# Kernel optimization log

Measured on AMD Instinct MI355X. Metric: run time of the kernel, lower is better.

The kernel has to match this reference:

```python
import jax, jax.numpy as jnp
import numpy as np

N = 50000      # nodes
E = 400000     # edges (before self-loops)
DIN = 128
HID = 128
HEADS = 4
DOUT = 64
NEG_SLOPE = 0.2  # PyG GATConv default


def setup_inputs() -> dict:
    key = jax.random.key(0)
    ks = jax.random.split(key, 14)

    def w(k, shape, fan_in):
        return jax.random.normal(k, shape, dtype=jnp.float32) * (1.0 / np.sqrt(fan_in))

    x = jax.random.normal(ks[0], (N, DIN), dtype=jnp.float32)
    edge_index = jax.random.randint(ks[1], (2, E), 0, N, dtype=jnp.int32)

    # layer 1: DIN -> HEADS*HID (concat)
    W1 = w(ks[2], (DIN, HEADS * HID), DIN)
    a_src1 = w(ks[3], (HEADS, HID), HID)
    a_dst1 = w(ks[4], (HEADS, HID), HID)
    b1 = jnp.zeros((HEADS * HID,), jnp.float32)
    # layer 2: HEADS*HID -> HEADS*HID (concat)
    W2 = w(ks[5], (HEADS * HID, HEADS * HID), HEADS * HID)
    a_src2 = w(ks[6], (HEADS, HID), HID)
    a_dst2 = w(ks[7], (HEADS, HID), HID)
    b2 = jnp.zeros((HEADS * HID,), jnp.float32)
    # layer 3: HEADS*HID -> DOUT, heads=1, concat=False (mean)
    W3 = w(ks[8], (HEADS * HID, DOUT), HEADS * HID)
    a_src3 = w(ks[9], (1, DOUT), DOUT)
    a_dst3 = w(ks[10], (1, DOUT), DOUT)
    b3 = jnp.zeros((DOUT,), jnp.float32)

    return dict(x=x, edge_index=edge_index,
                W1=W1, a_src1=a_src1, a_dst1=a_dst1, b1=b1,
                W2=W2, a_src2=a_src2, a_dst2=a_dst2, b2=b2,
                W3=W3, a_src3=a_src3, a_dst3=a_dst3, b3=b3)


def _gat_layer(x, src, dst, W, a_src, a_dst, n):
    """One GATConv (eval mode, self-loops already in src/dst). Returns [n, H, C]."""
    H, C = a_src.shape
    h = (x @ W).reshape(n, H, C)                        # projected features
    alpha_s = jnp.einsum('nhc,hc->nh', h, a_src)        # per-node src logits
    alpha_d = jnp.einsum('nhc,hc->nh', h, a_dst)
    e = jax.nn.leaky_relu(alpha_s[src] + alpha_d[dst], NEG_SLOPE)  # [E', H]
    # segment softmax over incoming edges of each dst node
    m = jax.ops.segment_max(e, dst, num_segments=n)
    e = jnp.exp(e - m[dst])
    s = jax.ops.segment_sum(e, dst, num_segments=n)
    alpha = e / (s[dst] + 1e-16)                        # [E', H]
    msg = h[src] * alpha[:, :, None]                    # [E', H, C]
    return jax.ops.segment_sum(msg, dst, num_segments=n)


def reference(x, edge_index, W1, a_src1, a_dst1, b1,
              W2, a_src2, a_dst2, b2, W3, a_src3, a_dst3, b3):
    n = x.shape[0]
    loops = jnp.arange(n, dtype=edge_index.dtype)       # PyG add_self_loops=True
    src = jnp.concatenate([edge_index[0], loops])
    dst = jnp.concatenate([edge_index[1], loops])

    h = _gat_layer(x, src, dst, W1, a_src1, a_dst1, n).reshape(n, -1) + b1
    h = jax.nn.elu(h)   # dropout is identity in eval mode
    h = _gat_layer(h, src, dst, W2, a_src2, a_dst2, n).reshape(n, -1) + b2
    h = jax.nn.elu(h)
    out = _gat_layer(h, src, dst, W3, a_src3, a_dst3, n)[:, 0, :] + b3  # heads=1, concat=False
    return out
```

## Files before the change

### kernel.cpp

```cpp
#include <hip/hip_runtime.h>
#include <hip/hip_bf16.h>


typedef __attribute__((ext_vector_type(8))) short bf16x8;
typedef __attribute__((ext_vector_type(4))) float f32x4;

__device__ __forceinline__ float bflo(unsigned w) { return __uint_as_float(w << 16); }
__device__ __forceinline__ float bfhi(unsigned w) { return __uint_as_float(w & 0xffff0000u); }
__device__ __forceinline__ float leaky(float x) { return x > 0.f ? x : 0.2f * x; }


__global__ void k_count(const int* __restrict__ ei, int E, int N, int* __restrict__ cnt) {
    int e = blockIdx.x * blockDim.x + threadIdx.x;
    int tot = E + N;
    if (e >= tot) return;
    int d = (e < E) ? ei[E + e] : (e - E);
    atomicAdd(&cnt[d], 1);
}

__global__ void k_scan1(const int* __restrict__ cnt, int N, int* __restrict__ rp,
                        int* __restrict__ blksum) {
    __shared__ int sdata[256];
    int t = threadIdx.x;
    int base = blockIdx.x * 1024;
    int v[4];
    int loc = 0;
#pragma unroll
    for (int i = 0; i < 4; i++) {
        int idx = base + t * 4 + i;
        v[i] = (idx < N) ? cnt[idx] : 0;
        loc += v[i];
    }
    int x = loc;
    sdata[t] = x;
    __syncthreads();
    for (int off = 1; off < 256; off <<= 1) {
        int y = (t >= off) ? sdata[t - off] : 0;
        __syncthreads();
        x += y;
        sdata[t] = x;
        __syncthreads();
    }
    int run = x - loc;
#pragma unroll
    for (int i = 0; i < 4; i++) {
        int idx = base + t * 4 + i;
        if (idx < N) rp[idx] = run;
        run += v[i];
    }
    if (t == 255) blksum[blockIdx.x] = x;
}

__global__ void k_scan2(const int* __restrict__ blksum, int nblk, int* __restrict__ blkoff) {
    int l = threadIdx.x;
    int v = (l < nblk) ? blksum[l] : 0;
    int x = v;
#pragma unroll
    for (int off = 1; off < 64; off <<= 1) {
        int y = __shfl_up(x, off);
        if (l >= off) x += y;
    }
    if (l < nblk) blkoff[l] = x - v;
}

__global__ void k_scan3(int* __restrict__ rp, const int* __restrict__ blkoff, int N, int Etot,
                        int* __restrict__ cur) {
    int i = blockIdx.x * blockDim.x + threadIdx.x;
    if (i < N) {
        int v = rp[i] + blkoff[i >> 10];
        rp[i] = v;
        cur[i] = v;
    }
    if (i == 0) rp[N] = Etot;
}

__global__ void k_fill(const int* __restrict__ ei, int E, int N, int* __restrict__ cur,
                       int* __restrict__ col, int* __restrict__ dste) {
    int e = blockIdx.x * blockDim.x + threadIdx.x;
    int tot = E + N;
    if (e >= tot) return;
    int s, d;
    if (e < E) { s = ei[e]; d = ei[E + e]; }
    else       { s = e - E; d = e - E; }
    int p = atomicAdd(&cur[d], 1);
    col[p] = s;
    dste[p] = d;
}


__global__ void k_cast_pad(const float* __restrict__ X, __hip_bfloat16* __restrict__ Xb,
                           int n_elems, int total) {
    int i = (blockIdx.x * blockDim.x + threadIdx.x) * 4;
    if (i >= total) return;
    float4 v = make_float4(0.f, 0.f, 0.f, 0.f);
    if (i < n_elems) v = *(const float4*)&X[i];
    __hip_bfloat16 tmp[4] = {__float2bfloat16(v.x), __float2bfloat16(v.y),
                             __float2bfloat16(v.z), __float2bfloat16(v.w)};
    *(ushort4*)&Xb[i] = *(const ushort4*)tmp;
}

__global__ void k_castT(const float* __restrict__ W, __hip_bfloat16* __restrict__ Wt,
                        int K, int Nw) {
    __shared__ float t[32][33];
    int k0 = blockIdx.x * 32, n0 = blockIdx.y * 32;
    int tx = threadIdx.x & 31, ty = threadIdx.x >> 5;
    for (int i = ty; i < 32; i += 8) t[i][tx] = W[(size_t)(k0 + i) * Nw + n0 + tx];
    __syncthreads();
    for (int i = ty; i < 32; i += 8)
        Wt[(size_t)(n0 + i) * K + k0 + tx] = __float2bfloat16(t[tx][i]);
}


template <int BN>
__global__ void __launch_bounds__(256) k_gemm_mfma(const __hip_bfloat16* __restrict__ A,
                                                   const __hip_bfloat16* __restrict__ Bt,
                                                   __hip_bfloat16* __restrict__ C,
                                                   int M, int Nn, int K) {
    constexpr int BM = 128, BK = 64;
    constexpr int WM = 64;
    constexpr int WN = BN / 2;
    constexpr int MREP = WM / 16;
    constexpr int NREP = WN / 16;

    __shared__ __hip_bfloat16 lds[(BM + BN) * BK];
    __hip_bfloat16* As = lds;
    __hip_bfloat16* Bs = lds + BM * BK;

    const int tid = threadIdx.x;
    const int wave = tid >> 6;
    const int lane = tid & 63;
    const int wm0 = (wave >> 1) * WM;
    const int wn0 = (wave & 1) * WN;
    const int m0 = blockIdx.y * BM;
    const int n0 = blockIdx.x * BN;
    const int fr = lane & 15;
    const int fq = lane >> 4;

    f32x4 acc[MREP][NREP] = {};

    for (int kt = 0; kt < K; kt += BK) {
        const __hip_bfloat16* srcA = A + (size_t)m0 * K + kt;
#pragma unroll
        for (int it = 0; it < BM * 8 / 256; ++it) {
            int gb = it * 256 + wave * 64;
            int g = gb + lane;
            int row = g >> 3;
            int kg = (g & 7) ^ (row & 7);
            const __hip_bfloat16* gsrc = srcA + (size_t)row * K + kg * 8;
            __builtin_amdgcn_global_load_lds(
                (const __attribute__((address_space(1))) void*)gsrc,
                (__attribute__((address_space(3))) void*)(As + gb * 8), 16, 0, 0);
        }
        const __hip_bfloat16* srcB = Bt + (size_t)n0 * K + kt;
#pragma unroll
        for (int it = 0; it < BN * 8 / 256; ++it) {
            int gb = it * 256 + wave * 64;
            int g = gb + lane;
            int row = g >> 3;
            int kg = (g & 7) ^ (row & 7);
            const __hip_bfloat16* gsrc = srcB + (size_t)row * K + kg * 8;
            __builtin_amdgcn_global_load_lds(
                (const __attribute__((address_space(1))) void*)gsrc,
                (__attribute__((address_space(3))) void*)(Bs + gb * 8), 16, 0, 0);
        }
        __syncthreads();

#pragma unroll
        for (int sl = 0; sl < 2; ++sl) {
            int ke = sl * 32 + fq * 8;
            bf16x8 af[MREP], bfr[NREP];
#pragma unroll
            for (int i = 0; i < MREP; ++i) {
                int row = wm0 + i * 16 + fr;
                int e = (row * BK + ke) ^ ((row & 7) << 3);
                af[i] = *(const bf16x8*)(As + e);
            }
#pragma unroll
            for (int j = 0; j < NREP; ++j) {
                int row = wn0 + j * 16 + fr;
                int e = (row * BK + ke) ^ ((row & 7) << 3);
                bfr[j] = *(const bf16x8*)(Bs + e);
            }
#pragma unroll
            for (int i = 0; i < MREP; ++i)
#pragma unroll
                for (int j = 0; j < NREP; ++j)
                    acc[i][j] = __builtin_amdgcn_mfma_f32_16x16x32_bf16(
                        af[i], bfr[j], acc[i][j], 0, 0, 0);
        }
        __syncthreads();
    }

#pragma unroll
    for (int i = 0; i < MREP; ++i) {
#pragma unroll
        for (int j = 0; j < NREP; ++j) {
            int col = n0 + wn0 + j * 16 + fr;
#pragma unroll
            for (int r = 0; r < 4; ++r) {
                int rowg = m0 + wm0 + i * 16 + fq * 4 + r;
                C[(size_t)rowg * Nn + col] = __float2bfloat16(acc[i][j][r]);
            }
        }
    }
}


template <int C, int H>
__global__ void k_alpha(const __hip_bfloat16* __restrict__ h, const float* __restrict__ a_src,
                        const float* __restrict__ a_dst, float* __restrict__ as_out,
                        float* __restrict__ ad_out, int N) {
    int w = (blockIdx.x * blockDim.x + threadIdx.x) >> 6;
    int lane = threadIdx.x & 63;
    int n = w / H, hd = w % H;
    if (n >= N) return;
    const __hip_bfloat16* hp = h + (size_t)n * (C * H) + hd * C;
    const float* asp = a_src + hd * C;
    const float* adp = a_dst + hd * C;
    float s1 = 0.f, s2 = 0.f;
    if constexpr (C == 128) {
        unsigned wrd = *(const unsigned*)(hp + 2 * lane);
        float f0 = bflo(wrd), f1 = bfhi(wrd);
        float2 a2 = *(const float2*)(asp + 2 * lane);
        float2 d2 = *(const float2*)(adp + 2 * lane);
        s1 = f0 * a2.x + f1 * a2.y;
        s2 = f0 * d2.x + f1 * d2.y;
    } else {
        float v = __bfloat162float(hp[lane & 63]);
        s1 = v * asp[lane];
        s2 = v * adp[lane];
    }
#pragma unroll
    for (int off = 32; off >= 1; off >>= 1) {
        s1 += __shfl_xor(s1, off);
        s2 += __shfl_xor(s2, off);
    }
    if (lane == 0) {
        as_out[n * H + hd] = s1;
        ad_out[n * H + hd] = s2;
    }
}


__global__ void k_nodestat4(const float* __restrict__ as, const float* __restrict__ ad,
                            const int* __restrict__ rp, const int* __restrict__ col,
                            float* __restrict__ mxb, float* __restrict__ invb, int N) {
    int n = blockIdx.x * blockDim.x + threadIdx.x;
    if (n >= N) return;
    int r0 = rp[n], r1 = rp[n + 1];
    float4 adv = *(const float4*)&ad[n * 4];
    float m0 = -1e30f, m1 = -1e30f, m2 = -1e30f, m3 = -1e30f;
    for (int e = r0; e < r1; e++) {
        int s = col[e];
        float4 a = *(const float4*)&as[s * 4];
        m0 = fmaxf(m0, leaky(a.x + adv.x));
        m1 = fmaxf(m1, leaky(a.y + adv.y));
        m2 = fmaxf(m2, leaky(a.z + adv.z));
        m3 = fmaxf(m3, leaky(a.w + adv.w));
    }
    float s0 = 0.f, s1 = 0.f, s2 = 0.f, s3 = 0.f;
    for (int e = r0; e < r1; e++) {
        int s = col[e];
        float4 a = *(const float4*)&as[s * 4];
        s0 += __expf(leaky(a.x + adv.x) - m0);
        s1 += __expf(leaky(a.y + adv.y) - m1);
        s2 += __expf(leaky(a.z + adv.z) - m2);
        s3 += __expf(leaky(a.w + adv.w) - m3);
    }
    *(float4*)&mxb[n * 4] = make_float4(m0, m1, m2, m3);
    *(float4*)&invb[n * 4] = make_float4(1.f / (s0 + 1e-16f), 1.f / (s1 + 1e-16f),
                                         1.f / (s2 + 1e-16f), 1.f / (s3 + 1e-16f));
}

__global__ void k_nodestat1(const float* __restrict__ as, const float* __restrict__ ad,
                            const int* __restrict__ rp, const int* __restrict__ col,
                            float* __restrict__ mxb, float* __restrict__ invb, int N) {
    int n = blockIdx.x * blockDim.x + threadIdx.x;
    if (n >= N) return;
    int r0 = rp[n], r1 = rp[n + 1];
    float adv = ad[n];
    float m0 = -1e30f;
    for (int e = r0; e < r1; e++) m0 = fmaxf(m0, leaky(as[col[e]] + adv));
    float s0 = 0.f;
    for (int e = r0; e < r1; e++) s0 += __expf(leaky(as[col[e]] + adv) - m0);
    mxb[n] = m0;
    invb[n] = 1.f / (s0 + 1e-16f);
}


__global__ void k_edgew4(const int* __restrict__ col, const int* __restrict__ dste,
                         const float* __restrict__ as, const float* __restrict__ ad,
                         const float* __restrict__ mxb, const float* __restrict__ invb,
                         float* __restrict__ wbuf, int Etot) {
    int e = blockIdx.x * blockDim.x + threadIdx.x;
    if (e >= Etot) return;
    int s = col[e], d = dste[e];
    float4 a = *(const float4*)&as[s * 4];
    float4 b = *(const float4*)&ad[d * 4];
    float4 m = *(const float4*)&mxb[d * 4];
    float4 iv = *(const float4*)&invb[d * 4];
    float4 w;
    w.x = __expf(leaky(a.x + b.x) - m.x) * iv.x;
    w.y = __expf(leaky(a.y + b.y) - m.y) * iv.y;
    w.z = __expf(leaky(a.z + b.z) - m.z) * iv.z;
    w.w = __expf(leaky(a.w + b.w) - m.w) * iv.w;
    *(float4*)&wbuf[e * 4] = w;
}

__global__ void k_edgew1(const int* __restrict__ col, const int* __restrict__ dste,
                         const float* __restrict__ as, const float* __restrict__ ad,
                         const float* __restrict__ mxb, const float* __restrict__ invb,
                         float* __restrict__ wbuf, int Etot) {
    int e = blockIdx.x * blockDim.x + threadIdx.x;
    if (e >= Etot) return;
    int s = col[e], d = dste[e];
    wbuf[e] = __expf(leaky(as[s] + ad[d]) - mxb[d]) * invb[d];
}


template <bool DO_ELU>
__global__ void k_gather512(const __hip_bfloat16* __restrict__ hfeat,
                            const float* __restrict__ wbuf, const int* __restrict__ rp,
                            const int* __restrict__ col, const float* __restrict__ bias,
                            __hip_bfloat16* __restrict__ out, int N) {
    int w = (blockIdx.x * blockDim.x + threadIdx.x) >> 6;
    int lane = threadIdx.x & 63;
    if (w >= N) return;
    int d = w;
    int r0 = rp[d], r1 = rp[d + 1];
    int hd_mine = lane >> 4;

    float acc[8] = {};
    int e = r0;
    for (; e + 1 < r1; e += 2) {
        int s0 = col[e], s1 = col[e + 1];
        float w0 = wbuf[e * 4 + hd_mine];
        float w1 = wbuf[e * 4 + 4 + hd_mine];
        uint4 v0 = *(const uint4*)(hfeat + (size_t)s0 * 512 + lane * 8);
        uint4 v1 = *(const uint4*)(hfeat + (size_t)s1 * 512 + lane * 8);
        acc[0] += w0 * bflo(v0.x); acc[1] += w0 * bfhi(v0.x);
        acc[2] += w0 * bflo(v0.y); acc[3] += w0 * bfhi(v0.y);
        acc[4] += w0 * bflo(v0.z); acc[5] += w0 * bfhi(v0.z);
        acc[6] += w0 * bflo(v0.w); acc[7] += w0 * bfhi(v0.w);
        acc[0] += w1 * bflo(v1.x); acc[1] += w1 * bfhi(v1.x);
        acc[2] += w1 * bflo(v1.y); acc[3] += w1 * bfhi(v1.y);
        acc[4] += w1 * bflo(v1.z); acc[5] += w1 * bfhi(v1.z);
        acc[6] += w1 * bflo(v1.w); acc[7] += w1 * bfhi(v1.w);
    }
    if (e < r1) {
        int s0 = col[e];
        float w0 = wbuf[e * 4 + hd_mine];
        uint4 v0 = *(const uint4*)(hfeat + (size_t)s0 * 512 + lane * 8);
        acc[0] += w0 * bflo(v0.x); acc[1] += w0 * bfhi(v0.x);
        acc[2] += w0 * bflo(v0.y); acc[3] += w0 * bfhi(v0.y);
        acc[4] += w0 * bflo(v0.z); acc[5] += w0 * bfhi(v0.z);
        acc[6] += w0 * bflo(v0.w); acc[7] += w0 * bfhi(v0.w);
    }

    __hip_bfloat16 tmp[8];
#pragma unroll
    for (int j = 0; j < 8; j++) {
        float v = acc[j] + bias[lane * 8 + j];
        if (DO_ELU) v = v > 0.f ? v : expm1f(v);
        tmp[j] = __float2bfloat16(v);
    }
    *(float4*)(out + (size_t)d * 512 + lane * 8) = *(const float4*)tmp;
}


__global__ void k_gather64(const __hip_bfloat16* __restrict__ hfeat,
                           const float* __restrict__ wbuf, const int* __restrict__ rp,
                           const int* __restrict__ col, const float* __restrict__ bias,
                           float* __restrict__ out, int N) {
    int w = (blockIdx.x * blockDim.x + threadIdx.x) >> 6;
    int lane = threadIdx.x & 63;
    if (w >= N) return;
    int d = w;
    int r0 = rp[d], r1 = rp[d + 1];
    int g = lane >> 4, cl = lane & 15;

    float a0 = 0.f, a1 = 0.f, a2 = 0.f, a3 = 0.f;
    for (int e0 = r0; e0 < r1; e0 += 4) {
        int e = e0 + g;
        bool valid = e < r1;
        int s = valid ? col[e] : 0;
        float wf = valid ? wbuf[e] : 0.f;
        uint2 q = *(const uint2*)(hfeat + (size_t)s * 64 + cl * 4);
        a0 += wf * bflo(q.x);
        a1 += wf * bfhi(q.x);
        a2 += wf * bflo(q.y);
        a3 += wf * bfhi(q.y);
    }
#pragma unroll
    for (int off = 16; off <= 32; off <<= 1) {
        a0 += __shfl_xor(a0, off);
        a1 += __shfl_xor(a1, off);
        a2 += __shfl_xor(a2, off);
        a3 += __shfl_xor(a3, off);
    }
    if (g == 0) {
        float4 b4 = *(const float4*)&bias[cl * 4];
        float4 o = make_float4(a0 + b4.x, a1 + b4.y, a2 + b4.z, a3 + b4.w);
        *(float4*)(out + (size_t)d * 64 + cl * 4) = o;
    }
}


extern "C" void kernel_launch(void* const* d_in, const int* in_sizes, int n_in,
                              void* d_out, int out_size, void* d_ws, size_t ws_size,
                              hipStream_t stream) {
    const float* x   = (const float*)d_in[0];
    const int*   ei  = (const int*)d_in[1];
    const float* W1  = (const float*)d_in[2];
    const float* as1 = (const float*)d_in[3];
    const float* ad1 = (const float*)d_in[4];
    const float* b1  = (const float*)d_in[5];
    const float* W2  = (const float*)d_in[6];
    const float* as2 = (const float*)d_in[7];
    const float* ad2 = (const float*)d_in[8];
    const float* b2  = (const float*)d_in[9];
    const float* W3  = (const float*)d_in[10];
    const float* as3 = (const float*)d_in[11];
    const float* ad3 = (const float*)d_in[12];
    const float* b3  = (const float*)d_in[13];

    const int N = in_sizes[0] / 128;
    const int E = in_sizes[1] / 2;
    const int Etot = E + N;
    const int Mp = (N + 127) & ~127;

    char* ws = (char*)d_ws;
    size_t off = 0;
    auto alloc = [&](size_t bytes) -> void* {
        void* p = ws + off;
        off = (off + bytes + 255) & ~(size_t)255;
        return p;
    };
    __hip_bfloat16* hbuf = (__hip_bfloat16*)alloc((size_t)Mp * 512 * 2);
    __hip_bfloat16* fbuf = (__hip_bfloat16*)alloc((size_t)Mp * 512 * 2);
    __hip_bfloat16* xb   = (__hip_bfloat16*)alloc((size_t)Mp * 128 * 2);
    __hip_bfloat16* Wt1  = (__hip_bfloat16*)alloc((size_t)512 * 128 * 2);
    __hip_bfloat16* Wt2  = (__hip_bfloat16*)alloc((size_t)512 * 512 * 2);
    __hip_bfloat16* Wt3  = (__hip_bfloat16*)alloc((size_t)64 * 512 * 2);
    float* aS   = (float*)alloc((size_t)N * 4 * 4);
    float* aD   = (float*)alloc((size_t)N * 4 * 4);
    float* mxb  = (float*)alloc((size_t)N * 4 * 4);
    float* invb = (float*)alloc((size_t)N * 4 * 4);
    float* wbuf = (float*)alloc((size_t)Etot * 4 * 4);
    int* cnt  = (int*)alloc((size_t)N * 4);
    int* rp   = (int*)alloc((size_t)(N + 1) * 4);
    int* cur  = (int*)alloc((size_t)N * 4);
    int* col  = (int*)alloc((size_t)Etot * 4);
    int* dste = (int*)alloc((size_t)Etot * 4);
    int* blks = (int*)alloc(64 * 4);
    int* blko = (int*)alloc(64 * 4);

    hipMemsetAsync(cnt, 0, (size_t)N * 4, stream);
    int thr = 256;
    k_count<<<(Etot + thr - 1) / thr, thr, 0, stream>>>(ei, E, N, cnt);
    int nblk = (N + 1023) / 1024;
    k_scan1<<<nblk, 256, 0, stream>>>(cnt, N, rp, blks);
    k_scan2<<<1, 64, 0, stream>>>(blks, nblk, blko);
    k_scan3<<<(N + 255) / 256, 256, 0, stream>>>(rp, blko, N, Etot, cur);
    k_fill<<<(Etot + thr - 1) / thr, thr, 0, stream>>>(ei, E, N, cur, col, dste);

    {
        int total = Mp * 128;
        k_cast_pad<<<(total / 4 + 255) / 256, 256, 0, stream>>>(x, xb, N * 128, total);
        dim3 g1(128 / 32, 512 / 32);
        k_castT<<<g1, 256, 0, stream>>>(W1, Wt1, 128, 512);
        dim3 g2(512 / 32, 512 / 32);
        k_castT<<<g2, 256, 0, stream>>>(W2, Wt2, 512, 512);
        dim3 g3(512 / 32, 64 / 32);
        k_castT<<<g3, 256, 0, stream>>>(W3, Wt3, 512, 64);
    }

    int alphaBlocks4 = (int)(((size_t)N * 4 * 64 + 255) / 256);
    int alphaBlocks1 = (int)(((size_t)N * 64 + 255) / 256);
    int nodeBlocks = (N + 255) / 256;
    int edgeBlocks = (Etot + 255) / 256;
    int gatBlocks = (N + 3) / 4;
    dim3 gemmG(512 / 128, Mp / 128);
    dim3 gemmG3(1, Mp / 128);

    k_gemm_mfma<128><<<gemmG, 256, 0, stream>>>(xb, Wt1, hbuf, Mp, 512, 128);
    k_alpha<128, 4><<<alphaBlocks4, 256, 0, stream>>>(hbuf, as1, ad1, aS, aD, N);
    k_nodestat4<<<nodeBlocks, 256, 0, stream>>>(aS, aD, rp, col, mxb, invb, N);
    k_edgew4<<<edgeBlocks, 256, 0, stream>>>(col, dste, aS, aD, mxb, invb, wbuf, Etot);
    k_gather512<true><<<gatBlocks, 256, 0, stream>>>(hbuf, wbuf, rp, col, b1, fbuf, N);

    k_gemm_mfma<128><<<gemmG, 256, 0, stream>>>(fbuf, Wt2, hbuf, Mp, 512, 512);
    k_alpha<128, 4><<<alphaBlocks4, 256, 0, stream>>>(hbuf, as2, ad2, aS, aD, N);
    k_nodestat4<<<nodeBlocks, 256, 0, stream>>>(aS, aD, rp, col, mxb, invb, N);
    k_edgew4<<<edgeBlocks, 256, 0, stream>>>(col, dste, aS, aD, mxb, invb, wbuf, Etot);
    k_gather512<true><<<gatBlocks, 256, 0, stream>>>(hbuf, wbuf, rp, col, b2, fbuf, N);

    k_gemm_mfma<64><<<gemmG3, 256, 0, stream>>>(fbuf, Wt3, hbuf, Mp, 64, 512);
    k_alpha<64, 1><<<alphaBlocks1, 256, 0, stream>>>(hbuf, as3, ad3, aS, aD, N);
    k_nodestat1<<<nodeBlocks, 256, 0, stream>>>(aS, aD, rp, col, mxb, invb, N);
    k_edgew1<<<edgeBlocks, 256, 0, stream>>>(col, dste, aS, aD, mxb, invb, wbuf, Etot);
    k_gather64<<<gatBlocks, 256, 0, stream>>>(hbuf, wbuf, rp, col, b3, (float*)d_out, N);
}
```

Baseline: 469.8 us.

## Drop max-subtraction softmax pass, defer normalization into padded CSR gather

Removes the per-node softmax statistics kernels: edge weights become plain exp(leaky(...)) without max subtraction, and the gather accumulates the weight sum and divides at the end. CSR rows are padded to multiples of four with zero-weight dummy edges, and edge weights are stored per head in a structure-of-arrays layout, so the gather can do aligned int4/float4 loads and unroll by four without tail handling. This cuts one kernel and two passes over edges per layer, at the cost of possible exp overflow when logits are large and some extra padded edges.

```diff
diff --git a/kernel.cpp b/kernel.cpp
--- a/kernel.cpp
+++ b/kernel.cpp
@@ -28,7 +28,7 @@
 #pragma unroll
     for (int i = 0; i < 4; i++) {
         int idx = base + t * 4 + i;
-        v[i] = (idx < N) ? cnt[idx] : 0;
+        v[i] = (idx < N) ? ((cnt[idx] + 3) & ~3) : 0;
         loc += v[i];
     }
     int x = loc;
@@ -63,7 +63,8 @@
     if (l < nblk) blkoff[l] = x - v;
 }
 
-__global__ void k_scan3(int* __restrict__ rp, const int* __restrict__ blkoff, int N, int Etot,
+__global__ void k_scan3(int* __restrict__ rp, const int* __restrict__ blkoff,
+                        const int* __restrict__ blksum, int N, int nblk,
                         int* __restrict__ cur) {
     int i = blockIdx.x * blockDim.x + threadIdx.x;
     if (i < N) {
@@ -71,7 +72,7 @@
         rp[i] = v;
         cur[i] = v;
     }
-    if (i == 0) rp[N] = Etot;
+    if (i == 0) rp[N] = blkoff[nblk - 1] + blksum[nblk - 1];
 }
 
 __global__ void k_fill(const int* __restrict__ ei, int E, int N, int* __restrict__ cur,
@@ -85,6 +86,18 @@
     int p = atomicAdd(&cur[d], 1);
     col[p] = s;
     dste[p] = d;
+}
+
+__global__ void k_padfill(const int* __restrict__ rp, const int* __restrict__ cnt, int N,
+                          int* __restrict__ col, int* __restrict__ dste) {
+    int n = blockIdx.x * blockDim.x + threadIdx.x;
+    if (n >= N) return;
+    int p = rp[n] + cnt[n];
+    int end = rp[n + 1];
+    for (; p < end; p++) {
+        col[p] = 0;
+        dste[p] = -1;
+    }
 }
 
 
@@ -242,79 +255,38 @@
 }
 
 
-__global__ void k_nodestat4(const float* __restrict__ as, const float* __restrict__ ad,
-                            const int* __restrict__ rp, const int* __restrict__ col,
-                            float* __restrict__ mxb, float* __restrict__ invb, int N) {
-    int n = blockIdx.x * blockDim.x + threadIdx.x;
-    if (n >= N) return;
-    int r0 = rp[n], r1 = rp[n + 1];
-    float4 adv = *(const float4*)&ad[n * 4];
-    float m0 = -1e30f, m1 = -1e30f, m2 = -1e30f, m3 = -1e30f;
-    for (int e = r0; e < r1; e++) {
-        int s = col[e];
-        float4 a = *(const float4*)&as[s * 4];
-        m0 = fmaxf(m0, leaky(a.x + adv.x));
-        m1 = fmaxf(m1, leaky(a.y + adv.y));
-        m2 = fmaxf(m2, leaky(a.z + adv.z));
-        m3 = fmaxf(m3, leaky(a.w + adv.w));
-    }
-    float s0 = 0.f, s1 = 0.f, s2 = 0.f, s3 = 0.f;
-    for (int e = r0; e < r1; e++) {
-        int s = col[e];
-        float4 a = *(const float4*)&as[s * 4];
-        s0 += __expf(leaky(a.x + adv.x) - m0);
-        s1 += __expf(leaky(a.y + adv.y) - m1);
-        s2 += __expf(leaky(a.z + adv.z) - m2);
-        s3 += __expf(leaky(a.w + adv.w) - m3);
-    }
-    *(float4*)&mxb[n * 4] = make_float4(m0, m1, m2, m3);
-    *(float4*)&invb[n * 4] = make_float4(1.f / (s0 + 1e-16f), 1.f / (s1 + 1e-16f),
-                                         1.f / (s2 + 1e-16f), 1.f / (s3 + 1e-16f));
-}
-
-__global__ void k_nodestat1(const float* __restrict__ as, const float* __restrict__ ad,
-                            const int* __restrict__ rp, const int* __restrict__ col,
-                            float* __restrict__ mxb, float* __restrict__ invb, int N) {
-    int n = blockIdx.x * blockDim.x + threadIdx.x;
-    if (n >= N) return;
-    int r0 = rp[n], r1 = rp[n + 1];
-    float adv = ad[n];
-    float m0 = -1e30f;
-    for (int e = r0; e < r1; e++) m0 = fmaxf(m0, leaky(as[col[e]] + adv));
-    float s0 = 0.f;
-    for (int e = r0; e < r1; e++) s0 += __expf(leaky(as[col[e]] + adv) - m0);
-    mxb[n] = m0;
-    invb[n] = 1.f / (s0 + 1e-16f);
-}
-
-
 __global__ void k_edgew4(const int* __restrict__ col, const int* __restrict__ dste,
                          const float* __restrict__ as, const float* __restrict__ ad,
-                         const float* __restrict__ mxb, const float* __restrict__ invb,
-                         float* __restrict__ wbuf, int Etot) {
+                         float* __restrict__ wbuf, const int* __restrict__ rp, int N, int EP) {
     int e = blockIdx.x * blockDim.x + threadIdx.x;
-    if (e >= Etot) return;
-    int s = col[e], d = dste[e];
+    int rpN = rp[N];
+    if (e >= rpN) return;
+    int d = dste[e];
+    if (d < 0) {
+        wbuf[e] = 0.f;
+        wbuf[EP + e] = 0.f;
+        wbuf[2 * EP + e] = 0.f;
+        wbuf[3 * EP + e] = 0.f;
+        return;
+    }
+    int s = col[e];
     float4 a = *(const float4*)&as[s * 4];
     float4 b = *(const float4*)&ad[d * 4];
-    float4 m = *(const float4*)&mxb[d * 4];
-    float4 iv = *(const float4*)&invb[d * 4];
-    float4 w;
-    w.x = __expf(leaky(a.x + b.x) - m.x) * iv.x;
-    w.y = __expf(leaky(a.y + b.y) - m.y) * iv.y;
-    w.z = __expf(leaky(a.z + b.z) - m.z) * iv.z;
-    w.w = __expf(leaky(a.w + b.w) - m.w) * iv.w;
-    *(float4*)&wbuf[e * 4] = w;
+    wbuf[e]          = __expf(leaky(a.x + b.x));
+    wbuf[EP + e]     = __expf(leaky(a.y + b.y));
+    wbuf[2 * EP + e] = __expf(leaky(a.z + b.z));
+    wbuf[3 * EP + e] = __expf(leaky(a.w + b.w));
 }
 
 __global__ void k_edgew1(const int* __restrict__ col, const int* __restrict__ dste,
                          const float* __restrict__ as, const float* __restrict__ ad,
-                         const float* __restrict__ mxb, const float* __restrict__ invb,
-                         float* __restrict__ wbuf, int Etot) {
+                         float* __restrict__ wbuf, const int* __restrict__ rp, int N) {
     int e = blockIdx.x * blockDim.x + threadIdx.x;
-    if (e >= Etot) return;
-    int s = col[e], d = dste[e];
-    wbuf[e] = __expf(leaky(as[s] + ad[d]) - mxb[d]) * invb[d];
+    int rpN = rp[N];
+    if (e >= rpN) return;
+    int d = dste[e];
+    if (d < 0) { wbuf[e] = 0.f; return; }
+    wbuf[e] = __expf(leaky(as[col[e]] + ad[d]));
 }
 
 
@@ -322,45 +294,47 @@
 __global__ void k_gather512(const __hip_bfloat16* __restrict__ hfeat,
                             const float* __restrict__ wbuf, const int* __restrict__ rp,
                             const int* __restrict__ col, const float* __restrict__ bias,
-                            __hip_bfloat16* __restrict__ out, int N) {
+                            __hip_bfloat16* __restrict__ out, int N, int EP) {
     int w = (blockIdx.x * blockDim.x + threadIdx.x) >> 6;
     int lane = threadIdx.x & 63;
     if (w >= N) return;
     int d = w;
     int r0 = rp[d], r1 = rp[d + 1];
-    int hd_mine = lane >> 4;
+    const float* wp = wbuf + (size_t)(lane >> 4) * EP;
 
     float acc[8] = {};
-    int e = r0;
-    for (; e + 1 < r1; e += 2) {
-        int s0 = col[e], s1 = col[e + 1];
-        float w0 = wbuf[e * 4 + hd_mine];
-        float w1 = wbuf[e * 4 + 4 + hd_mine];
-        uint4 v0 = *(const uint4*)(hfeat + (size_t)s0 * 512 + lane * 8);
-        uint4 v1 = *(const uint4*)(hfeat + (size_t)s1 * 512 + lane * 8);
-        acc[0] += w0 * bflo(v0.x); acc[1] += w0 * bfhi(v0.x);
-        acc[2] += w0 * bflo(v0.y); acc[3] += w0 * bfhi(v0.y);
-        acc[4] += w0 * bflo(v0.z); acc[5] += w0 * bfhi(v0.z);
-        acc[6] += w0 * bflo(v0.w); acc[7] += w0 * bfhi(v0.w);
-        acc[0] += w1 * bflo(v1.x); acc[1] += w1 * bfhi(v1.x);
-        acc[2] += w1 * bflo(v1.y); acc[3] += w1 * bfhi(v1.y);
-        acc[4] += w1 * bflo(v1.z); acc[5] += w1 * bfhi(v1.z);
-        acc[6] += w1 * bflo(v1.w); acc[7] += w1 * bfhi(v1.w);
-    }
-    if (e < r1) {
-        int s0 = col[e];
-        float w0 = wbuf[e * 4 + hd_mine];
-        uint4 v0 = *(const uint4*)(hfeat + (size_t)s0 * 512 + lane * 8);
-        acc[0] += w0 * bflo(v0.x); acc[1] += w0 * bfhi(v0.x);
-        acc[2] += w0 * bflo(v0.y); acc[3] += w0 * bfhi(v0.y);
-        acc[4] += w0 * bflo(v0.z); acc[5] += w0 * bfhi(v0.z);
-        acc[6] += w0 * bflo(v0.w); acc[7] += w0 * bfhi(v0.w);
-    }
-
+    float wsum = 0.f;
+    for (int e = r0; e < r1; e += 4) {
+        int4 c4 = *(const int4*)&col[e];
+        float4 w4 = *(const float4*)&wp[e];
+        uint4 v0 = *(const uint4*)(hfeat + (size_t)c4.x * 512 + lane * 8);
+        uint4 v1 = *(const uint4*)(hfeat + (size_t)c4.y * 512 + lane * 8);
+        uint4 v2 = *(const uint4*)(hfeat + (size_t)c4.z * 512 + lane * 8);
+        uint4 v3 = *(const uint4*)(hfeat + (size_t)c4.w * 512 + lane * 8);
+        wsum += (w4.x + w4.y) + (w4.z + w4.w);
+        acc[0] += w4.x * bflo(v0.x); acc[1] += w4.x * bfhi(v0.x);
+        acc[2] += w4.x * bflo(v0.y); acc[3] += w4.x * bfhi(v0.y);
+        acc[4] += w4.x * bflo(v0.z); acc[5] += w4.x * bfhi(v0.z);
+        acc[6] += w4.x * bflo(v0.w); acc[7] += w4.x * bfhi(v0.w);
+        acc[0] += w4.y * bflo(v1.x); acc[1] += w4.y * bfhi(v1.x);
+        acc[2] += w4.y * bflo(v1.y); acc[3] += w4.y * bfhi(v1.y);
+        acc[4] += w4.y * bflo(v1.z); acc[5] += w4.y * bfhi(v1.z);
+        acc[6] += w4.y * bflo(v1.w); acc[7] += w4.y * bfhi(v1.w);
+        acc[0] += w4.z * bflo(v2.x); acc[1] += w4.z * bfhi(v2.x);
+        acc[2] += w4.z * bflo(v2.y); acc[3] += w4.z * bfhi(v2.y);
+        acc[4] += w4.z * bflo(v2.z); acc[5] += w4.z * bfhi(v2.z);
+        acc[6] += w4.z * bflo(v2.w); acc[7] += w4.z * bfhi(v2.w);
+        acc[0] += w4.w * bflo(v3.x); acc[1] += w4.w * bfhi(v3.x);
+        acc[2] += w4.w * bflo(v3.y); acc[3] += w4.w * bfhi(v3.y);
+        acc[4] += w4.w * bflo(v3.z); acc[5] += w4.w * bfhi(v3.z);
+        acc[6] += w4.w * bflo(v3.w); acc[7] += w4.w * bfhi(v3.w);
+    }
+
+    float inv = 1.0f / (wsum + 1e-16f);
     __hip_bfloat16 tmp[8];
 #pragma unroll
     for (int j = 0; j < 8; j++) {
-        float v = acc[j] + bias[lane * 8 + j];
+        float v = acc[j] * inv + bias[lane * 8 + j];
         if (DO_ELU) v = v > 0.f ? v : expm1f(v);
         tmp[j] = __float2bfloat16(v);
     }
@@ -379,13 +353,13 @@
     int r0 = rp[d], r1 = rp[d + 1];
     int g = lane >> 4, cl = lane & 15;
 
-    float a0 = 0.f, a1 = 0.f, a2 = 0.f, a3 = 0.f;
+    float a0 = 0.f, a1 = 0.f, a2 = 0.f, a3 = 0.f, wsum = 0.f;
     for (int e0 = r0; e0 < r1; e0 += 4) {
         int e = e0 + g;
-        bool valid = e < r1;
-        int s = valid ? col[e] : 0;
-        float wf = valid ? wbuf[e] : 0.f;
+        int s = col[e];
+        float wf = wbuf[e];
         uint2 q = *(const uint2*)(hfeat + (size_t)s * 64 + cl * 4);
+        wsum += wf;
         a0 += wf * bflo(q.x);
         a1 += wf * bfhi(q.x);
         a2 += wf * bflo(q.y);
@@ -397,10 +371,13 @@
         a1 += __shfl_xor(a1, off);
         a2 += __shfl_xor(a2, off);
         a3 += __shfl_xor(a3, off);
+        wsum += __shfl_xor(wsum, off);
     }
     if (g == 0) {
+        float inv = 1.0f / (wsum + 1e-16f);
         float4 b4 = *(const float4*)&bias[cl * 4];
-        float4 o = make_float4(a0 + b4.x, a1 + b4.y, a2 + b4.z, a3 + b4.w);
+        float4 o = make_float4(a0 * inv + b4.x, a1 * inv + b4.y,
+                               a2 * inv + b4.z, a3 * inv + b4.w);
         *(float4*)(out + (size_t)d * 64 + cl * 4) = o;
     }
 }
@@ -427,6 +404,7 @@
     const int N = in_sizes[0] / 128;
     const int E = in_sizes[1] / 2;
     const int Etot = E + N;
+    const int EP = (Etot + 3 * N + 255) & ~255;
     const int Mp = (N + 127) & ~127;
 
     char* ws = (char*)d_ws;
@@ -444,14 +422,12 @@
     __hip_bfloat16* Wt3  = (__hip_bfloat16*)alloc((size_t)64 * 512 * 2);
     float* aS   = (float*)alloc((size_t)N * 4 * 4);
     float* aD   = (float*)alloc((size_t)N * 4 * 4);
-    float* mxb  = (float*)alloc((size_t)N * 4 * 4);
-    float* invb = (float*)alloc((size_t)N * 4 * 4);
-    float* wbuf = (float*)alloc((size_t)Etot * 4 * 4);
+    float* wbuf = (float*)alloc((size_t)EP * 4 * 4);
     int* cnt  = (int*)alloc((size_t)N * 4);
     int* rp   = (int*)alloc((size_t)(N + 1) * 4);
     int* cur  = (int*)alloc((size_t)N * 4);
-    int* col  = (int*)alloc((size_t)Etot * 4);
-    int* dste = (int*)alloc((size_t)Etot * 4);
+    int* col  = (int*)alloc((size_t)EP * 4);
+    int* dste = (int*)alloc((size_t)EP * 4);
     int* blks = (int*)alloc(64 * 4);
     int* blko = (int*)alloc(64 * 4);
 
@@ -461,8 +437,9 @@
     int nblk = (N + 1023) / 1024;
     k_scan1<<<nblk, 256, 0, stream>>>(cnt, N, rp, blks);
     k_scan2<<<1, 64, 0, stream>>>(blks, nblk, blko);
-    k_scan3<<<(N + 255) / 256, 256, 0, stream>>>(rp, blko, N, Etot, cur);
+    k_scan3<<<(N + 255) / 256, 256, 0, stream>>>(rp, blko, blks, N, nblk, cur);
     k_fill<<<(Etot + thr - 1) / thr, thr, 0, stream>>>(ei, E, N, cur, col, dste);
+    k_padfill<<<(N + 255) / 256, 256, 0, stream>>>(rp, cnt, N, col, dste);
 
     {
         int total = Mp * 128;
@@ -477,27 +454,23 @@
 
     int alphaBlocks4 = (int)(((size_t)N * 4 * 64 + 255) / 256);
     int alphaBlocks1 = (int)(((size_t)N * 64 + 255) / 256);
-    int nodeBlocks = (N + 255) / 256;
-    int edgeBlocks = (Etot + 255) / 256;
+    int edgeBlocks = (EP + 255) / 256;
     int gatBlocks = (N + 3) / 4;
     dim3 gemmG(512 / 128, Mp / 128);
     dim3 gemmG3(1, Mp / 128);
 
     k_gemm_mfma<128><<<gemmG, 256, 0, stream>>>(xb, Wt1, hbuf, Mp, 512, 128);
     k_alpha<128, 4><<<alphaBlocks4, 256, 0, stream>>>(hbuf, as1, ad1, aS, aD, N);
-    k_nodestat4<<<nodeBlocks, 256, 0, stream>>>(aS, aD, rp, col, mxb, invb, N);
-    k_edgew4<<<edgeBlocks, 256, 0, stream>>>(col, dste, aS, aD, mxb, invb, wbuf, Etot);
-    k_gather512<true><<<gatBlocks, 256, 0, stream>>>(hbuf, wbuf, rp, col, b1, fbuf, N);
+    k_edgew4<<<edgeBlocks, 256, 0, stream>>>(col, dste, aS, aD, wbuf, rp, N, EP);
+    k_gather512<true><<<gatBlocks, 256, 0, stream>>>(hbuf, wbuf, rp, col, b1, fbuf, N, EP);
 
     k_gemm_mfma<128><<<gemmG, 256, 0, stream>>>(fbuf, Wt2, hbuf, Mp, 512, 512);
     k_alpha<128, 4><<<alphaBlocks4, 256, 0, stream>>>(hbuf, as2, ad2, aS, aD, N);
-    k_nodestat4<<<nodeBlocks, 256, 0, stream>>>(aS, aD, rp, col, mxb, invb, N);
-    k_edgew4<<<edgeBlocks, 256, 0, stream>>>(col, dste, aS, aD, mxb, invb, wbuf, Etot);
-    k_gather512<true><<<gatBlocks, 256, 0, stream>>>(hbuf, wbuf, rp, col, b2, fbuf, N);
+    k_edgew4<<<edgeBlocks, 256, 0, stream>>>(col, dste, aS, aD, wbuf, rp, N, EP);
+    k_gather512<true><<<gatBlocks, 256, 0, stream>>>(hbuf, wbuf, rp, col, b2, fbuf, N, EP);
 
     k_gemm_mfma<64><<<gemmG3, 256, 0, stream>>>(fbuf, Wt3, hbuf, Mp, 64, 512);
     k_alpha<64, 1><<<alphaBlocks1, 256, 0, stream>>>(hbuf, as3, ad3, aS, aD, N);
-    k_nodestat1<<<nodeBlocks, 256, 0, stream>>>(aS, aD, rp, col, mxb, invb, N);
-    k_edgew1<<<edgeBlocks, 256, 0, stream>>>(col, dste, aS, aD, mxb, invb, wbuf, Etot);
+    k_edgew1<<<edgeBlocks, 256, 0, stream>>>(col, dste, aS, aD, wbuf, rp, N);
     k_gather64<<<gatBlocks, 256, 0, stream>>>(hbuf, wbuf, rp, col, b3, (float*)d_out, N);
 }
```

Measured after the change: 437.6 us. -6.9%, faster.
